# Kernel tuning notes

Hardware: AMD Instinct MI355X
Metric: run time of the kernel (lower is better)

The kernel has to match this reference:

```python
import jax, jax.numpy as jnp
import numpy as np

N_NODES = 8192
N_EDGES = 524288
N_PAIRS = 262144
N_TYPES = 86


def _gcn_conv(x, W, b, src, dst, n):
    # PyG GCNConv: transform, add self-loops, symmetric degree normalization,
    # scatter-add aggregation at destination nodes.
    xw = x @ W  # [N, F_out]
    loop = jnp.arange(n, dtype=src.dtype)
    s = jnp.concatenate([src, loop])
    d = jnp.concatenate([dst, loop])
    deg = jax.ops.segment_sum(jnp.ones(d.shape, xw.dtype), d, num_segments=n)
    dinv = jnp.where(deg > 0, jax.lax.rsqrt(deg), 0.0)  # deg^{-1/2}, 0 for isolated
    coef = dinv[s] * dinv[d]  # [E+N]
    out = jax.ops.segment_sum(xw[s] * coef[:, None], d, num_segments=n)
    return out + b


def setup_inputs() -> dict:
    key = jax.random.key(0)
    ks = jax.random.split(key, 10)
    x = jax.random.normal(ks[0], (N_NODES, N_NODES), dtype=jnp.float32)
    edge_index = jax.random.randint(ks[1], (2, N_EDGES), 0, N_NODES, dtype=jnp.int32)
    drug1_idx = jax.random.randint(ks[2], (N_PAIRS,), 0, N_NODES, dtype=jnp.int32)
    drug2_idx = jax.random.randint(ks[3], (N_PAIRS,), 0, N_NODES, dtype=jnp.int32)
    W1 = jax.random.normal(ks[4], (N_NODES, 128), dtype=jnp.float32) / np.sqrt(N_NODES)
    b1 = jnp.zeros((128,), jnp.float32)
    W2 = jax.random.normal(ks[5], (128, 64), dtype=jnp.float32) / np.sqrt(128.0)
    b2 = jnp.zeros((64,), jnp.float32)
    Wfc = jax.random.normal(ks[6], (128, N_TYPES), dtype=jnp.float32) / np.sqrt(128.0)
    bfc = jnp.zeros((N_TYPES,), jnp.float32)
    return {"x": x, "edge_index": edge_index, "drug1_idx": drug1_idx,
            "drug2_idx": drug2_idx, "W1": W1, "b1": b1, "W2": W2, "b2": b2,
            "Wfc": Wfc, "bfc": bfc}


def reference(x, edge_index, drug1_idx, drug2_idx, W1, b1, W2, b2, Wfc, bfc):
    n = x.shape[0]
    src, dst = edge_index[0], edge_index[1]
    h = jax.nn.relu(_gcn_conv(x, W1, b1, src, dst, n))
    # dropout p=0.3 is identity at inference (training=False)
    h = jax.nn.relu(_gcn_conv(h, W2, b2, src, dst, n))
    combined = jnp.concatenate([h[drug1_idx], h[drug2_idx]], axis=1)  # [P, 128]
    return jax.nn.sigmoid(combined @ Wfc + bfc)
```

## Files before the change

kernel.cpp:

```cpp
#include <hip/hip_runtime.h>
#include <math.h>
#include <stdint.h>
#include <stddef.h>

#define N_NODES 8192
#define N_EDGES 524288
#define N_PAIRS 262144
#define N_TYPES 86
#define F1 128
#define F2 64

typedef unsigned short ushort_t;
typedef unsigned int uint_t;
typedef __attribute__((ext_vector_type(8))) short bfrag;
typedef __attribute__((ext_vector_type(4))) float ffrag;

typedef __attribute__((address_space(3))) char lds_char;
typedef __attribute__((address_space(1))) const char g_char;

__device__ __forceinline__ void gload16(const void* g, void* l) {
  __builtin_amdgcn_global_load_lds((const g_char*)g, (lds_char*)l, 16, 0, 0);
}

__device__ inline ushort_t f2bf(float f) {
  uint_t u = __float_as_uint(f);
  uint_t r = u + 0x7fffu + ((u >> 16) & 1u);
  return (ushort_t)(r >> 16);
}
__device__ inline float bf2f(ushort_t h) {
  return __uint_as_float(((uint_t)h) << 16);
}


__global__ void zero_k(int* __restrict__ p) {
  p[blockIdx.x * 256 + threadIdx.x] = 0;
}

__global__ void count_deg_k(const int* __restrict__ dst, int* __restrict__ cnt) {
  int e = blockIdx.x * blockDim.x + threadIdx.x;
  if (e < N_EDGES) atomicAdd(&cnt[dst[e]], 1);
}

__global__ void dinv_k(const int* __restrict__ cnt, float* __restrict__ dinv) {
  int i = blockIdx.x * blockDim.x + threadIdx.x;
  if (i < N_NODES) dinv[i] = 1.0f / sqrtf((float)(cnt[i] + 1));
}

__global__ void scan_k(const int* __restrict__ cnt, int* __restrict__ rp,
                       int* __restrict__ fill) {
  __shared__ int s[1024];
  int t = threadIdx.x;
  int v[8];
  int sum = 0;
#pragma unroll
  for (int i = 0; i < 8; i++) { v[i] = cnt[t * 8 + i]; sum += v[i]; }
  s[t] = sum;
  __syncthreads();
  for (int off = 1; off < 1024; off <<= 1) {
    int add = (t >= off) ? s[t - off] : 0;
    __syncthreads();
    s[t] += add;
    __syncthreads();
  }
  int excl = s[t] - sum;
#pragma unroll
  for (int i = 0; i < 8; i++) {
    rp[t * 8 + i] = excl;
    fill[t * 8 + i] = excl;
    excl += v[i];
  }
  if (t == 1023) rp[N_NODES] = excl;
}

__global__ void scatter_k(const int* __restrict__ src, const int* __restrict__ dst,
                          int* fill, int* __restrict__ csr) {
  int e = blockIdx.x * blockDim.x + threadIdx.x;
  if (e < N_EDGES) {
    int d = dst[e];
    int pos = atomicAdd(&fill[d], 1);
    csr[pos] = src[e];
  }
}


__global__ __launch_bounds__(256) void w1split_k(const float* __restrict__ W1,
                                                 ushort_t* __restrict__ W1th,
                                                 ushort_t* __restrict__ W1tl) {
  __shared__ ushort_t lh[32 * 65];
  __shared__ ushort_t ll[32 * 65];
  int tid = threadIdx.x;
  int k0 = blockIdx.x * 64;
  int n0 = blockIdx.y * 32;
#pragma unroll
  for (int i = 0; i < 8; i++) {
    int c = tid + 256 * i;
    int kr = c >> 5, nc = c & 31;
    float v = W1[(size_t)(k0 + kr) * F1 + n0 + nc];
    ushort_t h = f2bf(v);
    ushort_t l = f2bf(v - bf2f(h));
    lh[nc * 65 + kr] = h;
    ll[nc * 65 + kr] = l;
  }
  __syncthreads();
#pragma unroll
  for (int i = 0; i < 2; i++) {
    int c = tid + 256 * i;
    int buf = c >> 8;
    int cc = c & 255;
    int nr = cc >> 3, kc = cc & 7;
    const ushort_t* l = buf ? ll : lh;
    uint4 u;
    u.x = (uint_t)l[nr * 65 + kc * 8 + 0] | ((uint_t)l[nr * 65 + kc * 8 + 1] << 16);
    u.y = (uint_t)l[nr * 65 + kc * 8 + 2] | ((uint_t)l[nr * 65 + kc * 8 + 3] << 16);
    u.z = (uint_t)l[nr * 65 + kc * 8 + 4] | ((uint_t)l[nr * 65 + kc * 8 + 5] << 16);
    u.w = (uint_t)l[nr * 65 + kc * 8 + 6] | ((uint_t)l[nr * 65 + kc * 8 + 7] << 16);
    ushort_t* dst = (buf ? W1tl : W1th) + (size_t)(n0 + nr) * N_NODES + k0 + kc * 8;
    *(uint4*)dst = u;
  }
}


#define BUFSZ 32768
#define OA_H 0
#define OA_L 8192
#define OB_H 16384
#define OB_L 24576

__global__ __launch_bounds__(256) void gemm1_mfma_k(const float* __restrict__ x,
                                                    const ushort_t* __restrict__ W1th,
                                                    const ushort_t* __restrict__ W1tl,
                                                    float* __restrict__ part, int kspan) {
  __shared__ __align__(16) char lds[2 * BUFSZ];
  int tid = threadIdx.x;
  int m_blk = blockIdx.y * 128;
  int kbase = blockIdx.x * kspan;
  int ktiles = kspan >> 5;
  int wave = tid >> 6, lane = tid & 63;
  int wr = wave >> 1, wc = wave & 1;
  int lrow = lane & 15, kgrp = lane >> 4;

  int b_rbase = wave * 16 + (lane >> 2);
  int b_kel = ((lane & 3) ^ ((lane >> 2) & 3)) * 8;

  ffrag acc[4][4];
#pragma unroll
  for (int mi = 0; mi < 4; mi++)
#pragma unroll
    for (int ni = 0; ni < 4; ni++) acc[mi][ni] = (ffrag)(0.0f);

  float4 av[4];

#define LOADA(K0)                                                                    \
  {                                                                                  \
    _Pragma("unroll") for (int i = 0; i < 4; i++) {                                  \
      int c = tid + 256 * i;                                                         \
      int row = c >> 3, c4 = c & 7;                                                  \
      av[i] = *(const float4*)&x[(size_t)(m_blk + row) * N_NODES + (K0) + 4 * c4];   \
    }                                                                                \
  }

#define LOADB(K0, BUFP)                                                              \
  {                                                                                  \
    _Pragma("unroll") for (int i = 0; i < 2; i++) {                                  \
      const ushort_t* gh = W1th + (size_t)(i * 64 + b_rbase) * N_NODES + (K0) + b_kel; \
      gload16(gh, (BUFP) + OB_H + i * 4096 + wave * 1024);                           \
      const ushort_t* gl = W1tl + (size_t)(i * 64 + b_rbase) * N_NODES + (K0) + b_kel; \
      gload16(gl, (BUFP) + OB_L + i * 4096 + wave * 1024);                           \
    }                                                                                \
  }

#define STOREA(BUFP)                                                                 \
  {                                                                                  \
    _Pragma("unroll") for (int i = 0; i < 4; i++) {                                  \
      int c = tid + 256 * i;                                                         \
      int row = c >> 3, c4 = c & 7;                                                  \
      float f0 = av[i].x, f1 = av[i].y, f2 = av[i].z, f3 = av[i].w;                  \
      ushort_t h0 = f2bf(f0), h1 = f2bf(f1), h2 = f2bf(f2), h3 = f2bf(f3);           \
      ushort_t l0 = f2bf(f0 - bf2f(h0)), l1 = f2bf(f1 - bf2f(h1));                   \
      ushort_t l2 = f2bf(f2 - bf2f(h2)), l3 = f2bf(f3 - bf2f(h3));                   \
      uint2 hp, lp;                                                                  \
      hp.x = (uint_t)h0 | ((uint_t)h1 << 16); hp.y = (uint_t)h2 | ((uint_t)h3 << 16);\
      lp.x = (uint_t)l0 | ((uint_t)l1 << 16); lp.y = (uint_t)l2 | ((uint_t)l3 << 16);\
      uint_t off = row * 64 + ((c4 * 8) ^ ((row & 3) << 4));                         \
      *(uint2*)((BUFP) + OA_H + off) = hp;                                           \
      *(uint2*)((BUFP) + OA_L + off) = lp;                                           \
    }                                                                                \
  }

#define COMPUTE(BUFP)                                                                \
  {                                                                                  \
    bfrag bh[4], bl[4];                                                              \
    _Pragma("unroll") for (int ni = 0; ni < 4; ni++) {                               \
      int brow = wc * 64 + ni * 16 + lrow;                                           \
      uint_t boff = brow * 64 + ((kgrp * 16) ^ ((brow & 3) << 4));                   \
      bh[ni] = *(const bfrag*)((BUFP) + OB_H + boff);                                \
      bl[ni] = *(const bfrag*)((BUFP) + OB_L + boff);                                \
    }                                                                                \
    _Pragma("unroll") for (int mi = 0; mi < 4; mi++) {                               \
      int arow = wr * 64 + mi * 16 + lrow;                                           \
      uint_t aoff = arow * 64 + ((kgrp * 16) ^ ((arow & 3) << 4));                   \
      bfrag ah = *(const bfrag*)((BUFP) + OA_H + aoff);                              \
      bfrag al = *(const bfrag*)((BUFP) + OA_L + aoff);                              \
      _Pragma("unroll") for (int ni = 0; ni < 4; ni++) {                             \
        acc[mi][ni] = __builtin_amdgcn_mfma_f32_16x16x32_bf16(ah, bh[ni], acc[mi][ni], 0, 0, 0); \
        acc[mi][ni] = __builtin_amdgcn_mfma_f32_16x16x32_bf16(ah, bl[ni], acc[mi][ni], 0, 0, 0); \
        acc[mi][ni] = __builtin_amdgcn_mfma_f32_16x16x32_bf16(al, bh[ni], acc[mi][ni], 0, 0, 0); \
      }                                                                              \
    }                                                                                \
  }

  LOADA(kbase);
  LOADB(kbase, lds);
  STOREA(lds);
  __syncthreads();

  int cur = 0;
  for (int kt = 0; kt < ktiles - 1; ++kt) {
    char* bufC = lds + cur * BUFSZ;
    char* bufN = lds + (cur ^ 1) * BUFSZ;
    int k0n = kbase + ((kt + 1) << 5);
    LOADA(k0n);
    LOADB(k0n, bufN);
    __builtin_amdgcn_sched_barrier(0);
    __builtin_amdgcn_s_setprio(1);
    COMPUTE(bufC);
    __builtin_amdgcn_s_setprio(0);
    STOREA(bufN);
    __syncthreads();
    cur ^= 1;
  }
  __builtin_amdgcn_s_setprio(1);
  COMPUTE(lds + cur * BUFSZ);
  __builtin_amdgcn_s_setprio(0);

  float* outp = part + (size_t)blockIdx.x * (N_NODES * F1);
#pragma unroll
  for (int mi = 0; mi < 4; mi++) {
#pragma unroll
    for (int ni = 0; ni < 4; ni++) {
      int col = wc * 64 + ni * 16 + lrow;
#pragma unroll
      for (int r = 0; r < 4; r++) {
        int row = m_blk + wr * 64 + mi * 16 + kgrp * 4 + r;
        outp[(size_t)row * F1 + col] = acc[mi][ni][r];
      }
    }
  }
#undef LOADA
#undef LOADB
#undef STOREA
#undef COMPUTE
}

__global__ void reduceS_k(const float* __restrict__ part, float* __restrict__ xw1, int S) {
  int i = blockIdx.x * blockDim.x + threadIdx.x;
  float4 a = ((const float4*)part)[i];
  for (int s = 1; s < S; s++) {
    float4 b = ((const float4*)(part + (size_t)s * N_NODES * F1))[i];
    a.x += b.x; a.y += b.y; a.z += b.z; a.w += b.w;
  }
  ((float4*)xw1)[i] = a;
}


template <int F>
__global__ void agg_k(const float* __restrict__ xw, const int* __restrict__ csr,
                      const int* __restrict__ rp, const float* __restrict__ dinv,
                      const float* __restrict__ bias, float* __restrict__ hout) {
  int node = blockIdx.x;
  int f = threadIdx.x;
  __shared__ int sidx[64];
  __shared__ float sdv[64];
  int beg = rp[node], end = rp[node + 1];
  float ax = 0.f, ay = 0.f;
  for (int base = beg; base < end; base += 64) {
    int n = end - base;
    if (n > 64) n = 64;
    __syncthreads();
    if (f < n) {
      int s = csr[base + f];
      sidx[f] = s;
      sdv[f] = dinv[s];
    }
    __syncthreads();
    if constexpr (F == 128) {
      for (int i = 0; i < n; i++) {
        float dv = sdv[i];
        float2 v = ((const float2*)&xw[(size_t)sidx[i] * F])[f];
        ax += v.x * dv;
        ay += v.y * dv;
      }
    } else {
      for (int i = 0; i < n; i++) ax += xw[(size_t)sidx[i] * F + f] * sdv[i];
    }
  }
  float dv = dinv[node];
  if constexpr (F == 128) {
    float2 sv = ((const float2*)&xw[(size_t)node * F])[f];
    float2 bb = ((const float2*)bias)[f];
    float vx = (ax + sv.x * dv) * dv + bb.x;
    float vy = (ay + sv.y * dv) * dv + bb.y;
    float2 o;
    o.x = vx > 0.f ? vx : 0.f;
    o.y = vy > 0.f ? vy : 0.f;
    ((float2*)&hout[(size_t)node * F])[f] = o;
  } else {
    float v = (ax + xw[(size_t)node * F + f] * dv) * dv + bias[f];
    hout[(size_t)node * F + f] = v > 0.f ? v : 0.f;
  }
}


__global__ __launch_bounds__(256) void gemm2_k(const float* __restrict__ h1,
                                               const float* __restrict__ W2,
                                               float* __restrict__ xw2) {
  __shared__ float W2s[F1 * F2];
  __shared__ float As[16 * F1];
  int tid = threadIdx.x;
  int r0 = blockIdx.x * 16;
#pragma unroll
  for (int j = 0; j < 8; j++)
    ((float4*)W2s)[tid + 256 * j] = ((const float4*)W2)[tid + 256 * j];
#pragma unroll
  for (int j = 0; j < 2; j++)
    ((float4*)As)[tid + 256 * j] = ((const float4*)(h1 + (size_t)r0 * F1))[tid + 256 * j];
  __syncthreads();
  int r = tid >> 4, c4 = tid & 15;
  float4 acc = make_float4(0.f, 0.f, 0.f, 0.f);
#pragma unroll 8
  for (int k = 0; k < F1; k++) {
    float a = As[r * F1 + k];
    float4 bv = *(float4*)&W2s[k * F2 + 4 * c4];
    acc.x += a * bv.x; acc.y += a * bv.y; acc.z += a * bv.z; acc.w += a * bv.w;
  }
  *(float4*)&xw2[(size_t)(r0 + r) * F2 + 4 * c4] = acc;
}


__global__ void pboth_k(const float* __restrict__ h2, const float* __restrict__ Wfc,
                        float* __restrict__ P) {
  __shared__ float hs[64 * 16];
  int tid = threadIdx.x;
  int r0 = blockIdx.x * 16;
  for (int idx = tid; idx < 256; idx += 192) {
    int row = idx >> 4, k4 = idx & 15;
    float4 h = *(const float4*)&h2[(size_t)(r0 + row) * F2 + 4 * k4];
    hs[(4 * k4 + 0) * 16 + row] = h.x;
    hs[(4 * k4 + 1) * 16 + row] = h.y;
    hs[(4 * k4 + 2) * 16 + row] = h.z;
    hs[(4 * k4 + 3) * 16 + row] = h.w;
  }
  __syncthreads();
  if (tid < 172) {
    int half = tid < 86 ? 0 : 1;
    int j = tid - 86 * half;
    const float* wp = Wfc + (size_t)(64 * half) * N_TYPES + j;
    float acc[16];
#pragma unroll
    for (int r = 0; r < 16; r++) acc[r] = 0.f;
    for (int k = 0; k < 64; k++) {
      float w = wp[(size_t)k * N_TYPES];
      const float* hk = &hs[k * 16];
#pragma unroll
      for (int r = 0; r < 16; r++) acc[r] += hk[r] * w;
    }
#pragma unroll
    for (int r = 0; r < 16; r++) P[(size_t)(r0 + r) * 172 + tid] = acc[r];
  }
}


__global__ void final_k(const float* __restrict__ P, const int* __restrict__ d1,
                        const int* __restrict__ d2, const float* __restrict__ bfc,
                        float* __restrict__ out) {
  int gid = blockIdx.x * blockDim.x + threadIdx.x;
  if (gid >= N_PAIRS * 43) return;
  int p = gid / 43;
  int j = gid - p * 43;
  int a = d1[p], b = d2[p];
  float2 v1 = *(const float2*)&P[(size_t)a * 172 + 2 * j];
  float2 v2 = *(const float2*)&P[(size_t)b * 172 + 86 + 2 * j];
  float2 bb = *(const float2*)&bfc[2 * j];
  float z0 = v1.x + v2.x + bb.x;
  float z1 = v1.y + v2.y + bb.y;
  float2 o;
  o.x = 1.0f / (1.0f + expf(-z0));
  o.y = 1.0f / (1.0f + expf(-z1));
  *(float2*)&out[(size_t)p * 86 + 2 * j] = o;
}


extern "C" void kernel_launch(void* const* d_in, const int* in_sizes, int n_in,
                              void* d_out, int out_size, void* d_ws, size_t ws_size,
                              hipStream_t stream) {
  const float* x   = (const float*)d_in[0];
  const int*   ei  = (const int*)d_in[1];
  const int*   d1  = (const int*)d_in[2];
  const int*   d2  = (const int*)d_in[3];
  const float* W1  = (const float*)d_in[4];
  const float* b1  = (const float*)d_in[5];
  const float* W2  = (const float*)d_in[6];
  const float* b2  = (const float*)d_in[7];
  const float* Wfc = (const float*)d_in[8];
  const float* bfc = (const float*)d_in[9];
  float* out = (float*)d_out;

  const int* esrc = ei;
  const int* edst = ei + N_EDGES;

  char* w = (char*)d_ws;
  size_t off = 0;
  auto alloc = [&](size_t bytes) -> char* {
    char* p = w + off;
    off += (bytes + 255) & ~(size_t)255;
    return p;
  };
  int*      cnt  = (int*)alloc((size_t)N_NODES * 4);
  float*    dinv = (float*)alloc((size_t)N_NODES * 4);
  int*      rp   = (int*)alloc((size_t)(N_NODES + 1) * 4);
  int*      fill = (int*)alloc((size_t)N_NODES * 4);
  int*      csr  = (int*)alloc((size_t)N_EDGES * 4);
  ushort_t* W1th = (ushort_t*)alloc((size_t)N_NODES * F1 * 2);
  ushort_t* W1tl = (ushort_t*)alloc((size_t)N_NODES * F1 * 2);
  float*    h1   = (float*)alloc((size_t)N_NODES * F1 * 4);
  float*    xw2  = (float*)alloc((size_t)N_NODES * F2 * 4);
  float*    h2   = (float*)alloc((size_t)N_NODES * F2 * 4);
  float*    P    = (float*)alloc((size_t)N_NODES * 172 * 4);

  size_t partBytes = (size_t)N_NODES * F1 * 4;
  int S = 8;
  while (S > 1 && off + (size_t)S * partBytes > ws_size) S >>= 1;
  float* part = (float*)alloc((size_t)S * partBytes);
  float* xw1 = part;
  if (off > ws_size) return;

  zero_k<<<N_NODES / 256, 256, 0, stream>>>(cnt);
  count_deg_k<<<N_EDGES / 256, 256, 0, stream>>>(edst, cnt);
  dinv_k<<<N_NODES / 256, 256, 0, stream>>>(cnt, dinv);
  scan_k<<<1, 1024, 0, stream>>>(cnt, rp, fill);
  scatter_k<<<N_EDGES / 256, 256, 0, stream>>>(esrc, edst, fill, csr);

  w1split_k<<<dim3(N_NODES / 64, F1 / 32), 256, 0, stream>>>(W1, W1th, W1tl);
  gemm1_mfma_k<<<dim3(S, N_NODES / 128), 256, 0, stream>>>(x, W1th, W1tl, part, N_NODES / S);
  if (S > 1)
    reduceS_k<<<(N_NODES * F1 / 4) / 256, 256, 0, stream>>>(part, xw1, S);
  agg_k<F1><<<N_NODES, 64, 0, stream>>>(xw1, csr, rp, dinv, b1, h1);

  gemm2_k<<<N_NODES / 16, 256, 0, stream>>>(h1, W2, xw2);
  agg_k<F2><<<N_NODES, 64, 0, stream>>>(xw2, csr, rp, dinv, b2, h2);

  pboth_k<<<N_NODES / 16, 192, 0, stream>>>(h2, Wfc, P);
  final_k<<<(N_PAIRS * 43) / 256, 256, 0, stream>>>(P, d1, d2, bfc, out);
}
```

Before: 274.4 us.

## Triple-buffer GEMM1 with 512-thread blocks, wave-per-node aggregation, fuse dinv into scan

```diff
diff --git a/kernel.cpp b/kernel.cpp
--- a/kernel.cpp
+++ b/kernel.cpp
@@ -41,19 +41,18 @@
   if (e < N_EDGES) atomicAdd(&cnt[dst[e]], 1);
 }
 
-__global__ void dinv_k(const int* __restrict__ cnt, float* __restrict__ dinv) {
-  int i = blockIdx.x * blockDim.x + threadIdx.x;
-  if (i < N_NODES) dinv[i] = 1.0f / sqrtf((float)(cnt[i] + 1));
-}
-
 __global__ void scan_k(const int* __restrict__ cnt, int* __restrict__ rp,
-                       int* __restrict__ fill) {
+                       int* __restrict__ fill, float* __restrict__ dinv) {
   __shared__ int s[1024];
   int t = threadIdx.x;
   int v[8];
   int sum = 0;
 #pragma unroll
-  for (int i = 0; i < 8; i++) { v[i] = cnt[t * 8 + i]; sum += v[i]; }
+  for (int i = 0; i < 8; i++) {
+    v[i] = cnt[t * 8 + i];
+    dinv[t * 8 + i] = 1.0f / sqrtf((float)(v[i] + 1));
+    sum += v[i];
+  }
   s[t] = sum;
   __syncthreads();
   for (int off = 1; off < 1024; off <<= 1) {
@@ -126,34 +125,37 @@
 #define OB_H 16384
 #define OB_L 24576
 
-__global__ __launch_bounds__(256) void gemm1_mfma_k(const float* __restrict__ x,
+__global__ __launch_bounds__(512) void gemm1_mfma_k(const float* __restrict__ x,
                                                     const ushort_t* __restrict__ W1th,
                                                     const ushort_t* __restrict__ W1tl,
                                                     float* __restrict__ part, int kspan) {
-  __shared__ __align__(16) char lds[2 * BUFSZ];
+  __shared__ __align__(16) char lds[3 * BUFSZ];
   int tid = threadIdx.x;
   int m_blk = blockIdx.y * 128;
   int kbase = blockIdx.x * kspan;
   int ktiles = kspan >> 5;
   int wave = tid >> 6, lane = tid & 63;
-  int wr = wave >> 1, wc = wave & 1;
+  int wr = wave >> 2, wc = wave & 3;
   int lrow = lane & 15, kgrp = lane >> 4;
 
-  int b_rbase = wave * 16 + (lane >> 2);
-  int b_kel = ((lane & 3) ^ ((lane >> 2) & 3)) * 8;
-
-  ffrag acc[4][4];
+  const ushort_t* bsrc = (wave < 4) ? W1th : W1tl;
+  int ob = (wave < 4) ? OB_H : OB_L;
+  int bq = (wave & 3);
+  int b_row = bq * 32 + (lane >> 2);
+  int b_kel = ((lane & 3) ^ ((lane >> 2) & 3)) << 3;
+
+  ffrag acc[4][2];
 #pragma unroll
   for (int mi = 0; mi < 4; mi++)
 #pragma unroll
-    for (int ni = 0; ni < 4; ni++) acc[mi][ni] = (ffrag)(0.0f);
-
-  float4 av[4];
+    for (int ni = 0; ni < 2; ni++) acc[mi][ni] = (ffrag)(0.0f);
+
+  float4 av[2];
 
 #define LOADA(K0)                                                                    \
   {                                                                                  \
-    _Pragma("unroll") for (int i = 0; i < 4; i++) {                                  \
-      int c = tid + 256 * i;                                                         \
+    _Pragma("unroll") for (int i = 0; i < 2; i++) {                                  \
+      int c = tid + 512 * i;                                                         \
       int row = c >> 3, c4 = c & 7;                                                  \
       av[i] = *(const float4*)&x[(size_t)(m_blk + row) * N_NODES + (K0) + 4 * c4];   \
     }                                                                                \
@@ -162,17 +164,15 @@
 #define LOADB(K0, BUFP)                                                              \
   {                                                                                  \
     _Pragma("unroll") for (int i = 0; i < 2; i++) {                                  \
-      const ushort_t* gh = W1th + (size_t)(i * 64 + b_rbase) * N_NODES + (K0) + b_kel; \
-      gload16(gh, (BUFP) + OB_H + i * 4096 + wave * 1024);                           \
-      const ushort_t* gl = W1tl + (size_t)(i * 64 + b_rbase) * N_NODES + (K0) + b_kel; \
-      gload16(gl, (BUFP) + OB_L + i * 4096 + wave * 1024);                           \
+      const ushort_t* gp = bsrc + (size_t)(b_row + i * 16) * N_NODES + (K0) + b_kel; \
+      gload16(gp, (BUFP) + ob + bq * 2048 + i * 1024);                               \
     }                                                                                \
   }
 
 #define STOREA(BUFP)                                                                 \
   {                                                                                  \
-    _Pragma("unroll") for (int i = 0; i < 4; i++) {                                  \
-      int c = tid + 256 * i;                                                         \
+    _Pragma("unroll") for (int i = 0; i < 2; i++) {                                  \
+      int c = tid + 512 * i;                                                         \
       int row = c >> 3, c4 = c & 7;                                                  \
       float f0 = av[i].x, f1 = av[i].y, f2 = av[i].z, f3 = av[i].w;                  \
       ushort_t h0 = f2bf(f0), h1 = f2bf(f1), h2 = f2bf(f2), h3 = f2bf(f3);           \
@@ -189,9 +189,9 @@
 
 #define COMPUTE(BUFP)                                                                \
   {                                                                                  \
-    bfrag bh[4], bl[4];                                                              \
-    _Pragma("unroll") for (int ni = 0; ni < 4; ni++) {                               \
-      int brow = wc * 64 + ni * 16 + lrow;                                           \
+    bfrag bh[2], bl[2];                                                              \
+    _Pragma("unroll") for (int ni = 0; ni < 2; ni++) {                               \
+      int brow = wc * 32 + ni * 16 + lrow;                                           \
       uint_t boff = brow * 64 + ((kgrp * 16) ^ ((brow & 3) << 4));                   \
       bh[ni] = *(const bfrag*)((BUFP) + OB_H + boff);                                \
       bl[ni] = *(const bfrag*)((BUFP) + OB_L + boff);                                \
@@ -201,7 +201,7 @@
       uint_t aoff = arow * 64 + ((kgrp * 16) ^ ((arow & 3) << 4));                   \
       bfrag ah = *(const bfrag*)((BUFP) + OA_H + aoff);                              \
       bfrag al = *(const bfrag*)((BUFP) + OA_L + aoff);                              \
-      _Pragma("unroll") for (int ni = 0; ni < 4; ni++) {                             \
+      _Pragma("unroll") for (int ni = 0; ni < 2; ni++) {                             \
         acc[mi][ni] = __builtin_amdgcn_mfma_f32_16x16x32_bf16(ah, bh[ni], acc[mi][ni], 0, 0, 0); \
         acc[mi][ni] = __builtin_amdgcn_mfma_f32_16x16x32_bf16(ah, bl[ni], acc[mi][ni], 0, 0, 0); \
         acc[mi][ni] = __builtin_amdgcn_mfma_f32_16x16x32_bf16(al, bh[ni], acc[mi][ni], 0, 0, 0); \
@@ -210,35 +210,50 @@
   }
 
   LOADA(kbase);
+  __builtin_amdgcn_sched_barrier(0);
   LOADB(kbase, lds);
+  asm volatile("s_waitcnt vmcnt(2)" ::: "memory");
+  __builtin_amdgcn_sched_barrier(0);
   STOREA(lds);
-  __syncthreads();
+  LOADA(kbase + 32);
+  __builtin_amdgcn_sched_barrier(0);
+  LOADB(kbase + 32, lds + BUFSZ);
+  asm volatile("s_waitcnt vmcnt(4) lgkmcnt(0)" ::: "memory");
+  __builtin_amdgcn_sched_barrier(0);
+  __builtin_amdgcn_s_barrier();
 
   int cur = 0;
-  for (int kt = 0; kt < ktiles - 1; ++kt) {
+  for (int kt = 0; kt < ktiles; ++kt) {
+    int nxt = cur + 1; if (nxt == 3) nxt = 0;
+    int nn2 = nxt + 1; if (nn2 == 3) nn2 = 0;
     char* bufC = lds + cur * BUFSZ;
-    char* bufN = lds + (cur ^ 1) * BUFSZ;
-    int k0n = kbase + ((kt + 1) << 5);
-    LOADA(k0n);
-    LOADB(k0n, bufN);
+    char* bufN = lds + nxt * BUFSZ;
+    char* bufNN = lds + nn2 * BUFSZ;
+    int knn = kt + 2; if (knn >= ktiles) knn = ktiles - 1;
+    int k0nn = kbase + (knn << 5);
+
+    asm volatile("s_waitcnt vmcnt(2)" ::: "memory");
+    __builtin_amdgcn_sched_barrier(0);
+    STOREA(bufN);
+    LOADA(k0nn);
+    __builtin_amdgcn_sched_barrier(0);
+    LOADB(k0nn, bufNN);
     __builtin_amdgcn_sched_barrier(0);
     __builtin_amdgcn_s_setprio(1);
     COMPUTE(bufC);
     __builtin_amdgcn_s_setprio(0);
-    STOREA(bufN);
-    __syncthreads();
-    cur ^= 1;
-  }
-  __builtin_amdgcn_s_setprio(1);
-  COMPUTE(lds + cur * BUFSZ);
-  __builtin_amdgcn_s_setprio(0);
+    asm volatile("s_waitcnt vmcnt(4) lgkmcnt(0)" ::: "memory");
+    __builtin_amdgcn_sched_barrier(0);
+    __builtin_amdgcn_s_barrier();
+    cur = nxt;
+  }
 
   float* outp = part + (size_t)blockIdx.x * (N_NODES * F1);
 #pragma unroll
   for (int mi = 0; mi < 4; mi++) {
 #pragma unroll
-    for (int ni = 0; ni < 4; ni++) {
-      int col = wc * 64 + ni * 16 + lrow;
+    for (int ni = 0; ni < 2; ni++) {
+      int col = wc * 32 + ni * 16 + lrow;
 #pragma unroll
       for (int r = 0; r < 4; r++) {
         int row = m_blk + wr * 64 + mi * 16 + kgrp * 4 + r;
@@ -264,42 +279,43 @@
 
 
 template <int F>
-__global__ void agg_k(const float* __restrict__ xw, const int* __restrict__ csr,
-                      const int* __restrict__ rp, const float* __restrict__ dinv,
-                      const float* __restrict__ bias, float* __restrict__ hout) {
-  int node = blockIdx.x;
-  int f = threadIdx.x;
-  __shared__ int sidx[64];
-  __shared__ float sdv[64];
+__global__ __launch_bounds__(256) void agg_k(const float* __restrict__ xw,
+                                             const int* __restrict__ csr,
+                                             const int* __restrict__ rp,
+                                             const float* __restrict__ dinv,
+                                             const float* __restrict__ bias,
+                                             float* __restrict__ hout) {
+  int node = blockIdx.x * 4 + (threadIdx.x >> 6);
+  int f = threadIdx.x & 63;
   int beg = rp[node], end = rp[node + 1];
   float ax = 0.f, ay = 0.f;
   for (int base = beg; base < end; base += 64) {
     int n = end - base;
     if (n > 64) n = 64;
-    __syncthreads();
+    int sv = 0;
+    float dvv = 0.f;
     if (f < n) {
-      int s = csr[base + f];
-      sidx[f] = s;
-      sdv[f] = dinv[s];
+      sv = csr[base + f];
+      dvv = dinv[sv];
     }
-    __syncthreads();
-    if constexpr (F == 128) {
-      for (int i = 0; i < n; i++) {
-        float dv = sdv[i];
-        float2 v = ((const float2*)&xw[(size_t)sidx[i] * F])[f];
+    for (int i = 0; i < n; i++) {
+      int s = __shfl(sv, i, 64);
+      float dv = __shfl(dvv, i, 64);
+      if constexpr (F == 128) {
+        float2 v = ((const float2*)&xw[(size_t)s * F])[f];
         ax += v.x * dv;
         ay += v.y * dv;
+      } else {
+        ax += xw[(size_t)s * F + f] * dv;
       }
-    } else {
-      for (int i = 0; i < n; i++) ax += xw[(size_t)sidx[i] * F + f] * sdv[i];
     }
   }
   float dv = dinv[node];
   if constexpr (F == 128) {
-    float2 sv = ((const float2*)&xw[(size_t)node * F])[f];
+    float2 sv2 = ((const float2*)&xw[(size_t)node * F])[f];
     float2 bb = ((const float2*)bias)[f];
-    float vx = (ax + sv.x * dv) * dv + bb.x;
-    float vy = (ay + sv.y * dv) * dv + bb.y;
+    float vx = (ax + sv2.x * dv) * dv + bb.x;
+    float vy = (ay + sv2.y * dv) * dv + bb.y;
     float2 o;
     o.x = vx > 0.f ? vx : 0.f;
     o.y = vy > 0.f ? vy : 0.f;
@@ -428,7 +444,7 @@
   float*    P    = (float*)alloc((size_t)N_NODES * 172 * 4);
 
   size_t partBytes = (size_t)N_NODES * F1 * 4;
-  int S = 8;
+  int S = 4;
   while (S > 1 && off + (size_t)S * partBytes > ws_size) S >>= 1;
   float* part = (float*)alloc((size_t)S * partBytes);
   float* xw1 = part;
@@ -436,19 +452,18 @@
 
   zero_k<<<N_NODES / 256, 256, 0, stream>>>(cnt);
   count_deg_k<<<N_EDGES / 256, 256, 0, stream>>>(edst, cnt);
-  dinv_k<<<N_NODES / 256, 256, 0, stream>>>(cnt, dinv);
-  scan_k<<<1, 1024, 0, stream>>>(cnt, rp, fill);
+  scan_k<<<1, 1024, 0, stream>>>(cnt, rp, fill, dinv);
   scatter_k<<<N_EDGES / 256, 256, 0, stream>>>(esrc, edst, fill, csr);
 
   w1split_k<<<dim3(N_NODES / 64, F1 / 32), 256, 0, stream>>>(W1, W1th, W1tl);
-  gemm1_mfma_k<<<dim3(S, N_NODES / 128), 256, 0, stream>>>(x, W1th, W1tl, part, N_NODES / S);
+  gemm1_mfma_k<<<dim3(S, N_NODES / 128), 512, 0, stream>>>(x, W1th, W1tl, part, N_NODES / S);
   if (S > 1)
     reduceS_k<<<(N_NODES * F1 / 4) / 256, 256, 0, stream>>>(part, xw1, S);
-  agg_k<F1><<<N_NODES, 64, 0, stream>>>(xw1, csr, rp, dinv, b1, h1);
+  agg_k<F1><<<N_NODES / 4, 256, 0, stream>>>(xw1, csr, rp, dinv, b1, h1);
 
   gemm2_k<<<N_NODES / 16, 256, 0, stream>>>(h1, W2, xw2);
-  agg_k<F2><<<N_NODES, 64, 0, stream>>>(xw2, csr, rp, dinv, b2, h2);
+  agg_k<F2><<<N_NODES / 4, 256, 0, stream>>>(xw2, csr, rp, dinv, b2, h2);
 
   pboth_k<<<N_NODES / 16, 192, 0, stream>>>(h2, Wfc, P);
-  final_k<<<(N_PAIRS * 43) / 256, 256, 0, stream>>>(P, d1, d2, bfc, out);
-}
+  final_k<<<(N_PAIRS * 43 + 255) / 256, 256, 0, stream>>>(P, d1, d2, bfc, out);
+}
```

Result: slower. 295.0 us (+7.5%).
